# Optimization experiments

Measured on AMD Instinct MI355X. Metric: run time of the kernel, lower is better.

Reference implementation:

```python
import jax, jax.numpy as jnp
import numpy as np

H = W = 512      # image spatial dims
C = 3            # channels
K = 32           # kernel size
S = 4            # stride
P = 10           # padding
THRESH = 0.5     # squared-L2 distance threshold
N_PATCH = (H + 2 * P - K) // S + 1  # 126 patches per dim
D = C * K * K    # 3072 patch feature dim


def setup_inputs() -> dict:
    key = jax.random.key(0)
    k1, k2, k3, k4 = jax.random.split(key, 4)
    image = jax.random.uniform(k1, (H, W, C), dtype=jnp.float32)
    mem = jax.random.normal(k2, (4096, D), dtype=jnp.float32)
    mem2 = jax.random.normal(k3, (4096, D), dtype=jnp.float32)
    mapping = jax.random.randint(k4, (4096,), 0, 4096, dtype=jnp.int64)
    return {"image": image, "mem": mem, "mem2": mem2, "mapping": mapping}


def _unfold(img_chw):
    # torch.nn.functional.unfold: -> [L, C*K*K] with feature order (c, kh, kw)
    padded = jnp.pad(img_chw, ((0, 0), (P, P), (P, P)))
    r = (jnp.arange(N_PATCH) * S)[:, None] + jnp.arange(K)[None, :]  # [nH, K]
    c = (jnp.arange(N_PATCH) * S)[:, None] + jnp.arange(K)[None, :]  # [nW, K]
    # patches: [C, nH, nW, K, K]
    patches = padded[:, r[:, None, :, None], c[None, :, None, :]]
    patches = patches.transpose(1, 2, 0, 3, 4)  # [nH, nW, C, K, K]
    return patches.reshape(N_PATCH * N_PATCH, D)


def _fold(patches_ld):
    # inverse of _unfold: scatter-add overlapping patches, crop padding
    p5 = patches_ld.reshape(N_PATCH, N_PATCH, C, K, K)
    r = (jnp.arange(N_PATCH) * S)[:, None] + jnp.arange(K)[None, :]
    c = (jnp.arange(N_PATCH) * S)[:, None] + jnp.arange(K)[None, :]
    canvas = jnp.zeros((C, H + 2 * P, W + 2 * P), dtype=patches_ld.dtype)
    ci = jnp.arange(C)[None, None, :, None, None]
    ri = r[:, None, None, :, None]
    cci = c[None, :, None, None, :]
    canvas = canvas.at[ci, ri, cci].add(p5)
    return canvas[:, P:P + H, P:P + W]  # [C, H, W]


def reference(image, mem, mem2, mapping):
    img_chw = image.transpose(2, 0, 1)            # [C, H, W]
    u = _unfold(img_chw)                           # [L, D]
    # brute-force squared-L2 1-NN against mem bank (FAISS IndexFlatL2)
    d2 = (jnp.sum(u * u, axis=1, keepdims=True)
          - 2.0 * (u @ mem.T)
          + jnp.sum(mem * mem, axis=1)[None, :])   # [L, N]
    dmin = jnp.min(d2, axis=1)                     # [L]
    idx = jnp.argmin(d2, axis=1)                   # [L]
    # counter-based pattern lookup: mem id -> mem2 pattern id -> reconstruct
    recon = mem2[mapping[idx]]                     # [L, D]
    out_p = jnp.where(dmin[:, None] >= THRESH, u, recon)
    folded = _fold(out_p)                          # [C, H, W]
    out = folded / jnp.max(folded)
    return out.transpose(1, 2, 0)                  # [H, W, C]
```

## Files before the change

### kernel.cpp

```cpp
#include <hip/hip_runtime.h>
#include <stdint.h>

#define HH 512
#define WW 512
#define CC 3
#define KK 32
#define SS 4
#define PP 10
#define NPATCH 126
#define NP2 (NPATCH * NPATCH)
#define DD 3072
#define NMEM 4096
#define THRESHV 0.5f

#define OFF_NORMS  0
#define OFF_CNT    4096
#define OFF_FAIL   4352
#define OFF_PMAXA  20480
#define OFF_PMAXB  21504

__device__ inline float wave_max(float v) {
    for (int off = 32; off; off >>= 1) v = fmaxf(v, __shfl_xor(v, off, 64));
    return v;
}
__device__ inline float wave_min(float v) {
    for (int off = 32; off; off >>= 1) v = fminf(v, __shfl_xor(v, off, 64));
    return v;
}
__device__ inline float wave_sum(float v) {
    for (int off = 32; off; off >>= 1) v += __shfl_xor(v, off, 64);
    return v;
}
__device__ inline int wave_sum_i(int v) {
    for (int off = 32; off; off >>= 1) v += __shfl_xor(v, off, 64);
    return v;
}

__device__ inline int cov1(int v) {
    int pv = v + PP;
    int a = pv - (KK - 1);
    int imin = (a <= 0) ? 0 : ((a + SS - 1) >> 2);
    int imax = pv >> 2;
    if (imax > NPATCH - 1) imax = NPATCH - 1;
    return imax - imin + 1;
}

__global__ void norms_fold(const float* __restrict__ mem,
                           const float* __restrict__ img,
                           float* __restrict__ norms,
                           float* __restrict__ pmaxA,
                           float* __restrict__ out) {
    __shared__ float smx[4];
    int b = blockIdx.x, tid = threadIdx.x;
    int lane = tid & 63, w = tid >> 6;

    float m = -INFINITY;
    if (tid < 192) {
        int f = b * 192 + tid;
        float4 v = ((const float4*)img)[f];
        float r[4] = {v.x, v.y, v.z, v.w};
        int e = f * 4;
#pragma unroll
        for (int k = 0; k < 4; ++k) {
            int px = (e + k) / 3;
            int y = px >> 9, x = px & 511;
            float cv = (float)(cov1(y) * cov1(x));
            r[k] *= cv;
            m = fmaxf(m, r[k]);
        }
        float4 o; o.x = r[0]; o.y = r[1]; o.z = r[2]; o.w = r[3];
        ((float4*)out)[f] = o;
    }

    int row = b * 4 + w;
    const float4* rp = (const float4*)(mem + (size_t)row * DD);
    float4 v[12];
#pragma unroll
    for (int i = 0; i < 12; ++i) v[i] = rp[lane + (i << 6)];
    float s0 = 0.f, s1 = 0.f, s2 = 0.f, s3 = 0.f;
#pragma unroll
    for (int i = 0; i < 12; ++i) {
        s0 += v[i].x * v[i].x; s1 += v[i].y * v[i].y;
        s2 += v[i].z * v[i].z; s3 += v[i].w * v[i].w;
    }
    float s = wave_sum((s0 + s1) + (s2 + s3));
    if (lane == 0) norms[row] = s;

    m = wave_max(m);
    if (lane == 0) smx[w] = m;
    __syncthreads();
    if (tid == 0)
        pmaxA[b] = fmaxf(fmaxf(smx[0], smx[1]), fmaxf(smx[2], smx[3]));
}

__global__ void patch_cert(const float* __restrict__ img,
                           const float* __restrict__ norms,
                           uint32_t* __restrict__ counts,
                           uint32_t* __restrict__ fails) {
    __shared__ float cs[WW];
    __shared__ float red[16];
    __shared__ float s_mn, s_mx;
    __shared__ uint32_t s_cnt;
    __shared__ uint32_t s_list[NPATCH];
    int py = blockIdx.x;
    int tid = threadIdx.x;
    int lane = tid & 63, w = tid >> 6;

    if (tid == 0) s_cnt = 0;

    float mn = INFINITY, mx = -INFINITY;
#pragma unroll
    for (int k = 0; k < 8; ++k) {
        float v = norms[tid + (k << 9)];
        mn = fminf(mn, v); mx = fmaxf(mx, v);
    }
    mn = wave_min(mn); mx = wave_max(mx);
    if (lane == 0) { red[w] = mn; red[8 + w] = mx; }
    __syncthreads();
    if (tid == 0) {
        float a = INFINITY, bmx = -INFINITY;
#pragma unroll
        for (int k = 0; k < 8; ++k) {
            a = fminf(a, red[k]); bmx = fmaxf(bmx, red[8 + k]);
        }
        s_mn = sqrtf(a); s_mx = sqrtf(bmx);
    }

    int y0 = py * SS - PP;
    float s = 0.f;
#pragma unroll
    for (int ky = 0; ky < KK; ++ky) {
        int y = y0 + ky;
        if (y >= 0 && y < HH) {
            const float* p = img + ((size_t)y * WW + tid) * CC;
            s += p[0] * p[0] + p[1] * p[1] + p[2] * p[2];
        }
    }
    cs[tid] = s;
    __syncthreads();

    if (tid < NPATCH) {
        int x0 = tid * SS - PP;
        float t = 0.f;
#pragma unroll
        for (int kx = 0; kx < KK; ++kx) {
            int xx = x0 + kx;
            if (xx >= 0 && xx < WW) t += cs[xx];
        }
        float un = sqrtf(t);
        float gap = 0.f;
        if (un <= s_mn) gap = s_mn - un;
        else if (un >= s_mx) gap = un - s_mx;
        if (gap * gap < THRESHV) {
            uint32_t pos = atomicAdd(&s_cnt, 1u);
            s_list[pos] = (uint32_t)(py * NPATCH + tid);
        }
    }
    __syncthreads();
    uint32_t c = s_cnt;
    if (tid == 0) counts[py] = c;
    if (tid < c) fails[py * 128 + tid] = s_list[tid];
}

__global__ void fallback_fix(const float* __restrict__ img,
                             const float* __restrict__ mem,
                             const float* __restrict__ mem2,
                             const int* __restrict__ mapping,
                             const uint32_t* __restrict__ counts,
                             const uint32_t* __restrict__ fails,
                             float* __restrict__ out) {
    __shared__ float smin[256];
    __shared__ int   sarg[256];
    int seq = 0;
    for (int py = 0; py < NPATCH; ++py) {
        uint32_t cnt = counts[py];
        for (uint32_t e = 0; e < cnt; ++e, ++seq) {
            if ((uint32_t)(seq % gridDim.x) != blockIdx.x) continue;
            int patch = (int)fails[py * 128 + e];
            int pi = patch / NPATCH, pj = patch % NPATCH;
            int y0 = pi * SS - PP, x0 = pj * SS - PP;
            float best = INFINITY; int barg = NMEM;
            for (int j = threadIdx.x; j < NMEM; j += blockDim.x) {
                const float* mr = mem + (size_t)j * DD;
                float s = 0.f;
                for (int d = 0; d < DD; ++d) {
                    int c = d >> 10, rem = d & 1023, ky = rem >> 5, kx = rem & 31;
                    int y = y0 + ky, x = x0 + kx;
                    float u = (y >= 0 && y < HH && x >= 0 && x < WW)
                                  ? img[((size_t)y * WW + x) * CC + c] : 0.f;
                    float dif = u - mr[d];
                    s += dif * dif;
                }
                if (s < best) { best = s; barg = j; }
            }
            smin[threadIdx.x] = best; sarg[threadIdx.x] = barg;
            __syncthreads();
            for (int stride = 128; stride; stride >>= 1) {
                if ((int)threadIdx.x < stride) {
                    float s2 = smin[threadIdx.x + stride];
                    int   a2 = sarg[threadIdx.x + stride];
                    if (s2 < smin[threadIdx.x] ||
                        (s2 == smin[threadIdx.x] && a2 < sarg[threadIdx.x])) {
                        smin[threadIdx.x] = s2; sarg[threadIdx.x] = a2;
                    }
                }
                __syncthreads();
            }
            float dmin = smin[0]; int arg = sarg[0];
            if (dmin < THRESHV) {
                const float* rec = mem2 + (size_t)mapping[arg] * DD;
                for (int d = threadIdx.x; d < DD; d += blockDim.x) {
                    int c = d >> 10, rem = d & 1023, ky = rem >> 5, kx = rem & 31;
                    int y = y0 + ky, x = x0 + kx;
                    if (y >= 0 && y < HH && x >= 0 && x < WW) {
                        float u = img[((size_t)y * WW + x) * CC + c];
                        atomicAdd(&out[((size_t)y * WW + x) * CC + c],
                                  rec[d] - u);
                    }
                }
            }
            __syncthreads();
        }
    }
}

__global__ void rescan_max(const uint32_t* __restrict__ counts,
                           const float* __restrict__ out,
                           float* __restrict__ pmaxB) {
    __shared__ int sneed[4];
    __shared__ float smx[4];
    int tid = threadIdx.x, lane = tid & 63, w = tid >> 6;
    int c = (tid < NPATCH) ? (int)counts[tid] : 0;
    c = wave_sum_i(c);
    if (lane == 0) sneed[w] = c;
    __syncthreads();
    int need = sneed[0] + sneed[1] + sneed[2] + sneed[3];
    if (need == 0) return;
    float m = -INFINITY;
    if (tid < 192) {
        int f = blockIdx.x * 192 + tid;
        float4 v = ((const float4*)out)[f];
        m = fmaxf(fmaxf(v.x, v.y), fmaxf(v.z, v.w));
    }
    m = wave_max(m);
    if (lane == 0) smx[w] = m;
    __syncthreads();
    if (tid == 0)
        pmaxB[blockIdx.x] = fmaxf(fmaxf(smx[0], smx[1]), fmaxf(smx[2], smx[3]));
}

__global__ void normalize_k(const uint32_t* __restrict__ counts,
                            const float* __restrict__ pmaxA,
                            const float* __restrict__ pmaxB,
                            float* __restrict__ out) {
    __shared__ int sneed[4];
    __shared__ float smx[4];
    __shared__ float s_inv;
    int tid = threadIdx.x, lane = tid & 63, w = tid >> 6;
    int c = (tid < NPATCH) ? (int)counts[tid] : 0;
    c = wave_sum_i(c);
    if (lane == 0) sneed[w] = c;
    __syncthreads();
    int need = sneed[0] + sneed[1] + sneed[2] + sneed[3];
    const float* pm = need ? pmaxB : pmaxA;
    float m = -INFINITY;
#pragma unroll
    for (int k = 0; k < 4; ++k) m = fmaxf(m, pm[tid + (k << 8)]);
    m = wave_max(m);
    if (lane == 0) smx[w] = m;
    __syncthreads();
    if (tid == 0)
        s_inv = 1.0f / fmaxf(fmaxf(smx[0], smx[1]), fmaxf(smx[2], smx[3]));
    __syncthreads();
    float inv = s_inv;
    float4* o4 = (float4*)out;
    int base = blockIdx.x * 768 + tid;
#pragma unroll
    for (int k = 0; k < 3; ++k) {
        int f = base + (k << 8);
        float4 v = o4[f];
        v.x *= inv; v.y *= inv; v.z *= inv; v.w *= inv;
        o4[f] = v;
    }
}

extern "C" void kernel_launch(void* const* d_in, const int* in_sizes, int n_in,
                              void* d_out, int out_size, void* d_ws, size_t ws_size,
                              hipStream_t stream) {
    const float* img     = (const float*)d_in[0];
    const float* mem     = (const float*)d_in[1];
    const float* mem2    = (const float*)d_in[2];
    const int*   mapping = (const int*)d_in[3];
    float* out    = (float*)d_out;
    uint32_t* wsu = (uint32_t*)d_ws;

    float*    norms  = (float*)(wsu + OFF_NORMS);
    uint32_t* counts = wsu + OFF_CNT;
    uint32_t* fails  = wsu + OFF_FAIL;
    float*    pmaxA  = (float*)(wsu + OFF_PMAXA);
    float*    pmaxB  = (float*)(wsu + OFF_PMAXB);

    norms_fold <<<1024, 256, 0, stream>>>(mem, img, norms, pmaxA, out);
    patch_cert <<<NPATCH, 512, 0, stream>>>(img, norms, counts, fails);
    fallback_fix<<<64, 256, 0, stream>>>(img, mem, mem2, mapping, counts,
                                         fails, out);
    rescan_max <<<1024, 256, 0, stream>>>(counts, out, pmaxB);
    normalize_k<<<256, 256, 0, stream>>>(counts, pmaxA, pmaxB, out);
}
```

Before: 143.7 us.

## Fuse patch-norm computation into first kernel and certification into fallback kernel

Patch-norm computation moves into extra blocks of the norms/fold kernel, so it runs alongside the memory-bank norm pass. The certification check now runs inside the fallback kernel, where each block scans a contiguous range of patches. This removes one launch and the separate counts/fails lists. Each fallback block now redoes the 4096-entry min/max reduction and loops serially over about 248 patches, which adds per-block work in exchange for fewer launches.

```diff
diff --git a/kernel.cpp b/kernel.cpp
--- a/kernel.cpp
+++ b/kernel.cpp
@@ -14,10 +14,10 @@
 #define THRESHV 0.5f
 
 #define OFF_NORMS  0
-#define OFF_CNT    4096
-#define OFF_FAIL   4352
-#define OFF_PMAXA  20480
-#define OFF_PMAXB  21504
+#define OFF_PNORM  4096
+#define OFF_MODCNT 20480
+#define OFF_PMAXA  36864
+#define OFF_PMAXB  37888
 
 __device__ inline float wave_max(float v) {
     for (int off = 32; off; off >>= 1) v = fmaxf(v, __shfl_xor(v, off, 64));
@@ -28,10 +28,6 @@
     return v;
 }
 __device__ inline float wave_sum(float v) {
-    for (int off = 32; off; off >>= 1) v += __shfl_xor(v, off, 64);
-    return v;
-}
-__device__ inline int wave_sum_i(int v) {
     for (int off = 32; off; off >>= 1) v += __shfl_xor(v, off, 64);
     return v;
 }
@@ -45,14 +41,49 @@
     return imax - imin + 1;
 }
 
-__global__ void norms_fold(const float* __restrict__ mem,
+__global__ void fused_main(const float* __restrict__ mem,
                            const float* __restrict__ img,
                            float* __restrict__ norms,
+                           float* __restrict__ pnorm,
                            float* __restrict__ pmaxA,
                            float* __restrict__ out) {
+    __shared__ float cs[WW];
     __shared__ float smx[4];
     int b = blockIdx.x, tid = threadIdx.x;
     int lane = tid & 63, w = tid >> 6;
+
+    if (b >= 1024) {
+        int py = b - 1024;
+        if (py >= NPATCH) return;
+        int y0 = py * SS - PP;
+        float s0 = 0.f, s1 = 0.f;
+        int x0c = tid, x1c = tid + 256;
+#pragma unroll
+        for (int ky = 0; ky < KK; ++ky) {
+            int y = y0 + ky;
+            if (y >= 0 && y < HH) {
+                const float* row = img + (size_t)y * WW * CC;
+                const float* p0 = row + x0c * CC;
+                const float* p1 = row + x1c * CC;
+                s0 += p0[0] * p0[0] + p0[1] * p0[1] + p0[2] * p0[2];
+                s1 += p1[0] * p1[0] + p1[1] * p1[1] + p1[2] * p1[2];
+            }
+        }
+        cs[x0c] = s0;
+        cs[x1c] = s1;
+        __syncthreads();
+        if (tid < NPATCH) {
+            int x0 = tid * SS - PP;
+            float t = 0.f;
+#pragma unroll
+            for (int kx = 0; kx < KK; ++kx) {
+                int xx = x0 + kx;
+                if (xx >= 0 && xx < WW) t += cs[xx];
+            }
+            pnorm[py * NPATCH + tid] = t;
+        }
+        return;
+    }
 
     float m = -INFINITY;
     if (tid < 192) {
@@ -93,149 +124,113 @@
         pmaxA[b] = fmaxf(fmaxf(smx[0], smx[1]), fmaxf(smx[2], smx[3]));
 }
 
-__global__ void patch_cert(const float* __restrict__ img,
-                           const float* __restrict__ norms,
-                           uint32_t* __restrict__ counts,
-                           uint32_t* __restrict__ fails) {
-    __shared__ float cs[WW];
-    __shared__ float red[16];
+__global__ void cert_fix(const float* __restrict__ img,
+                         const float* __restrict__ mem,
+                         const float* __restrict__ mem2,
+                         const int* __restrict__ mapping,
+                         const float* __restrict__ norms,
+                         const float* __restrict__ pnorm,
+                         float* __restrict__ out,
+                         uint32_t* __restrict__ modcnt) {
+    __shared__ float rmn[4], rmx[4];
     __shared__ float s_mn, s_mx;
-    __shared__ uint32_t s_cnt;
-    __shared__ uint32_t s_list[NPATCH];
-    int py = blockIdx.x;
-    int tid = threadIdx.x;
-    int lane = tid & 63, w = tid >> 6;
-
-    if (tid == 0) s_cnt = 0;
-
-    float mn = INFINITY, mx = -INFINITY;
-#pragma unroll
-    for (int k = 0; k < 8; ++k) {
-        float v = norms[tid + (k << 9)];
-        mn = fminf(mn, v); mx = fmaxf(mx, v);
-    }
-    mn = wave_min(mn); mx = wave_max(mx);
-    if (lane == 0) { red[w] = mn; red[8 + w] = mx; }
-    __syncthreads();
-    if (tid == 0) {
-        float a = INFINITY, bmx = -INFINITY;
-#pragma unroll
-        for (int k = 0; k < 8; ++k) {
-            a = fminf(a, red[k]); bmx = fmaxf(bmx, red[8 + k]);
-        }
-        s_mn = sqrtf(a); s_mx = sqrtf(bmx);
-    }
-
-    int y0 = py * SS - PP;
-    float s = 0.f;
-#pragma unroll
-    for (int ky = 0; ky < KK; ++ky) {
-        int y = y0 + ky;
-        if (y >= 0 && y < HH) {
-            const float* p = img + ((size_t)y * WW + tid) * CC;
-            s += p[0] * p[0] + p[1] * p[1] + p[2] * p[2];
-        }
-    }
-    cs[tid] = s;
-    __syncthreads();
-
-    if (tid < NPATCH) {
-        int x0 = tid * SS - PP;
-        float t = 0.f;
-#pragma unroll
-        for (int kx = 0; kx < KK; ++kx) {
-            int xx = x0 + kx;
-            if (xx >= 0 && xx < WW) t += cs[xx];
-        }
-        float un = sqrtf(t);
-        float gap = 0.f;
-        if (un <= s_mn) gap = s_mn - un;
-        else if (un >= s_mx) gap = un - s_mx;
-        if (gap * gap < THRESHV) {
-            uint32_t pos = atomicAdd(&s_cnt, 1u);
-            s_list[pos] = (uint32_t)(py * NPATCH + tid);
-        }
-    }
-    __syncthreads();
-    uint32_t c = s_cnt;
-    if (tid == 0) counts[py] = c;
-    if (tid < c) fails[py * 128 + tid] = s_list[tid];
-}
-
-__global__ void fallback_fix(const float* __restrict__ img,
-                             const float* __restrict__ mem,
-                             const float* __restrict__ mem2,
-                             const int* __restrict__ mapping,
-                             const uint32_t* __restrict__ counts,
-                             const uint32_t* __restrict__ fails,
-                             float* __restrict__ out) {
     __shared__ float smin[256];
     __shared__ int   sarg[256];
-    int seq = 0;
-    for (int py = 0; py < NPATCH; ++py) {
-        uint32_t cnt = counts[py];
-        for (uint32_t e = 0; e < cnt; ++e, ++seq) {
-            if ((uint32_t)(seq % gridDim.x) != blockIdx.x) continue;
-            int patch = (int)fails[py * 128 + e];
-            int pi = patch / NPATCH, pj = patch % NPATCH;
-            int y0 = pi * SS - PP, x0 = pj * SS - PP;
-            float best = INFINITY; int barg = NMEM;
-            for (int j = threadIdx.x; j < NMEM; j += blockDim.x) {
-                const float* mr = mem + (size_t)j * DD;
-                float s = 0.f;
-                for (int d = 0; d < DD; ++d) {
-                    int c = d >> 10, rem = d & 1023, ky = rem >> 5, kx = rem & 31;
-                    int y = y0 + ky, x = x0 + kx;
-                    float u = (y >= 0 && y < HH && x >= 0 && x < WW)
-                                  ? img[((size_t)y * WW + x) * CC + c] : 0.f;
-                    float dif = u - mr[d];
-                    s += dif * dif;
+    __shared__ int   s_mod;
+    int tid = threadIdx.x, lane = tid & 63, w = tid >> 6;
+    if (tid == 0) s_mod = 0;
+
+    float mn = INFINITY, mx = -INFINITY;
+#pragma unroll
+    for (int k = 0; k < 16; ++k) {
+        float v = norms[tid + (k << 8)];
+        mn = fminf(mn, v); mx = fmaxf(mx, v);
+    }
+    mn = wave_min(mn); mx = wave_max(mx);
+    if (lane == 0) { rmn[w] = mn; rmx[w] = mx; }
+    __syncthreads();
+    if (tid == 0) {
+        s_mn = sqrtf(fminf(fminf(rmn[0], rmn[1]), fminf(rmn[2], rmn[3])));
+        s_mx = sqrtf(fmaxf(fmaxf(rmx[0], rmx[1]), fmaxf(rmx[2], rmx[3])));
+    }
+    __syncthreads();
+    float lo = s_mn, hi = s_mx;
+
+    int per = (NP2 + gridDim.x - 1) / gridDim.x;
+    int p0 = blockIdx.x * per;
+    int p1 = p0 + per; if (p1 > NP2) p1 = NP2;
+    for (int p = p0; p < p1; ++p) {
+        float un = sqrtf(pnorm[p]);
+        float gap = 0.f;
+        if (un <= lo) gap = lo - un;
+        else if (un >= hi) gap = un - hi;
+        if (gap * gap >= THRESHV) continue;
+
+        int pi = p / NPATCH, pj = p % NPATCH;
+        int y0 = pi * SS - PP, x0 = pj * SS - PP;
+        float best = INFINITY; int barg = NMEM;
+        for (int j = tid; j < NMEM; j += 256) {
+            const float* mr = mem + (size_t)j * DD;
+            float sacc = 0.f;
+            for (int d = 0; d < DD; ++d) {
+                int c = d >> 10, rem = d & 1023, ky = rem >> 5, kx = rem & 31;
+                int y = y0 + ky, x = x0 + kx;
+                float u = (y >= 0 && y < HH && x >= 0 && x < WW)
+                              ? img[((size_t)y * WW + x) * CC + c] : 0.f;
+                float dif = u - mr[d];
+                sacc += dif * dif;
+            }
+            if (sacc < best) { best = sacc; barg = j; }
+        }
+        smin[tid] = best; sarg[tid] = barg;
+        __syncthreads();
+        for (int stride = 128; stride; stride >>= 1) {
+            if (tid < stride) {
+                float s2 = smin[tid + stride];
+                int   a2 = sarg[tid + stride];
+                if (s2 < smin[tid] || (s2 == smin[tid] && a2 < sarg[tid])) {
+                    smin[tid] = s2; sarg[tid] = a2;
                 }
-                if (s < best) { best = s; barg = j; }
-            }
-            smin[threadIdx.x] = best; sarg[threadIdx.x] = barg;
+            }
             __syncthreads();
-            for (int stride = 128; stride; stride >>= 1) {
-                if ((int)threadIdx.x < stride) {
-                    float s2 = smin[threadIdx.x + stride];
-                    int   a2 = sarg[threadIdx.x + stride];
-                    if (s2 < smin[threadIdx.x] ||
-                        (s2 == smin[threadIdx.x] && a2 < sarg[threadIdx.x])) {
-                        smin[threadIdx.x] = s2; sarg[threadIdx.x] = a2;
-                    }
+        }
+        float dmin = smin[0]; int arg = sarg[0];
+        if (dmin < THRESHV) {
+            const float* rec = mem2 + (size_t)mapping[arg] * DD;
+            for (int d = tid; d < DD; d += 256) {
+                int c = d >> 10, rem = d & 1023, ky = rem >> 5, kx = rem & 31;
+                int y = y0 + ky, x = x0 + kx;
+                if (y >= 0 && y < HH && x >= 0 && x < WW) {
+                    float u = img[((size_t)y * WW + x) * CC + c];
+                    atomicAdd(&out[((size_t)y * WW + x) * CC + c],
+                              rec[d] - u);
                 }
-                __syncthreads();
-            }
-            float dmin = smin[0]; int arg = sarg[0];
-            if (dmin < THRESHV) {
-                const float* rec = mem2 + (size_t)mapping[arg] * DD;
-                for (int d = threadIdx.x; d < DD; d += blockDim.x) {
-                    int c = d >> 10, rem = d & 1023, ky = rem >> 5, kx = rem & 31;
-                    int y = y0 + ky, x = x0 + kx;
-                    if (y >= 0 && y < HH && x >= 0 && x < WW) {
-                        float u = img[((size_t)y * WW + x) * CC + c];
-                        atomicAdd(&out[((size_t)y * WW + x) * CC + c],
-                                  rec[d] - u);
-                    }
-                }
-            }
-            __syncthreads();
-        }
-    }
-}
-
-__global__ void rescan_max(const uint32_t* __restrict__ counts,
-                           const float* __restrict__ out,
-                           float* __restrict__ pmaxB) {
-    __shared__ int sneed[4];
+            }
+            if (tid == 0) s_mod++;
+        }
+        __syncthreads();
+    }
+    __syncthreads();
+    if (tid == 0) modcnt[blockIdx.x] = (uint32_t)s_mod;
+}
+
+__global__ void rescan_pmax(const uint32_t* __restrict__ modcnt,
+                            const float* __restrict__ pmaxA,
+                            const float* __restrict__ out,
+                            float* __restrict__ pmaxB) {
+    __shared__ int s_need;
     __shared__ float smx[4];
     int tid = threadIdx.x, lane = tid & 63, w = tid >> 6;
-    int c = (tid < NPATCH) ? (int)counts[tid] : 0;
-    c = wave_sum_i(c);
-    if (lane == 0) sneed[w] = c;
-    __syncthreads();
-    int need = sneed[0] + sneed[1] + sneed[2] + sneed[3];
-    if (need == 0) return;
+    if (w == 0) {
+        int c = (int)modcnt[lane];
+        for (int off = 32; off; off >>= 1) c += __shfl_xor(c, off, 64);
+        if (lane == 0) s_need = c;
+    }
+    __syncthreads();
+    if (s_need == 0) {
+        if (tid == 0) pmaxB[blockIdx.x] = pmaxA[blockIdx.x];
+        return;
+    }
     float m = -INFINITY;
     if (tid < 192) {
         int f = blockIdx.x * 192 + tid;
@@ -249,23 +244,14 @@
         pmaxB[blockIdx.x] = fmaxf(fmaxf(smx[0], smx[1]), fmaxf(smx[2], smx[3]));
 }
 
-__global__ void normalize_k(const uint32_t* __restrict__ counts,
-                            const float* __restrict__ pmaxA,
-                            const float* __restrict__ pmaxB,
+__global__ void normalize_k(const float* __restrict__ pmaxB,
                             float* __restrict__ out) {
-    __shared__ int sneed[4];
     __shared__ float smx[4];
     __shared__ float s_inv;
     int tid = threadIdx.x, lane = tid & 63, w = tid >> 6;
-    int c = (tid < NPATCH) ? (int)counts[tid] : 0;
-    c = wave_sum_i(c);
-    if (lane == 0) sneed[w] = c;
-    __syncthreads();
-    int need = sneed[0] + sneed[1] + sneed[2] + sneed[3];
-    const float* pm = need ? pmaxB : pmaxA;
     float m = -INFINITY;
 #pragma unroll
-    for (int k = 0; k < 4; ++k) m = fmaxf(m, pm[tid + (k << 8)]);
+    for (int k = 0; k < 4; ++k) m = fmaxf(m, pmaxB[tid + (k << 8)]);
     m = wave_max(m);
     if (lane == 0) smx[w] = m;
     __syncthreads();
@@ -295,15 +281,14 @@
     uint32_t* wsu = (uint32_t*)d_ws;
 
     float*    norms  = (float*)(wsu + OFF_NORMS);
-    uint32_t* counts = wsu + OFF_CNT;
-    uint32_t* fails  = wsu + OFF_FAIL;
+    float*    pnorm  = (float*)(wsu + OFF_PNORM);
+    uint32_t* modcnt = wsu + OFF_MODCNT;
     float*    pmaxA  = (float*)(wsu + OFF_PMAXA);
     float*    pmaxB  = (float*)(wsu + OFF_PMAXB);
 
-    norms_fold <<<1024, 256, 0, stream>>>(mem, img, norms, pmaxA, out);
-    patch_cert <<<NPATCH, 512, 0, stream>>>(img, norms, counts, fails);
-    fallback_fix<<<64, 256, 0, stream>>>(img, mem, mem2, mapping, counts,
-                                         fails, out);
-    rescan_max <<<1024, 256, 0, stream>>>(counts, out, pmaxB);
-    normalize_k<<<256, 256, 0, stream>>>(counts, pmaxA, pmaxB, out);
-}
+    fused_main <<<1152, 256, 0, stream>>>(mem, img, norms, pnorm, pmaxA, out);
+    cert_fix   <<<64, 256, 0, stream>>>(img, mem, mem2, mapping, norms,
+                                        pnorm, out, modcnt);
+    rescan_pmax<<<1024, 256, 0, stream>>>(modcnt, pmaxA, out, pmaxB);
+    normalize_k<<<256, 256, 0, stream>>>(pmaxB, out);
+}
```

New measurement: 173.8 us. 20.9% more time.
